# Kernel optimization log

Hardware: AMD Instinct MI355X
Metric: run time of the kernel (lower is better)

Reference implementation:

```python
import jax, jax.numpy as jnp
import numpy as np

B, T, DM, H, DH = 4, 2048, 1024, 16, 64
DI = H * DH
CLIP = 1.0
LN_EPS = 1e-5


def setup_inputs() -> dict:
    key = jax.random.key(0)
    ks = jax.random.split(key, 9)

    def xav(k, shape):  # xavier_uniform, fan_in=shape[1], fan_out=shape[0]
        lim = float(np.sqrt(6.0 / (shape[0] + shape[1])))
        return jax.random.uniform(k, shape, jnp.float32, -lim, lim)

    def kai(k, shape):  # default nn.Linear weight init
        lim = float(1.0 / np.sqrt(shape[1]))
        return jax.random.uniform(k, shape, jnp.float32, -lim, lim)

    return {
        "x": jax.random.normal(ks[0], (B, T, DM), jnp.float32),
        "Wq": xav(ks[1], (DI, DM)),
        "Wk": xav(ks[2], (DI, DM)),
        "Wv": xav(ks[3], (DI, DM)),
        "Wa": kai(ks[4], (DI, DM)), "ba": jnp.full((DI,), 3.0, jnp.float32),
        "Wb": kai(ks[5], (H, DM)), "bb": jnp.zeros((H,), jnp.float32),
        "Wg": kai(ks[6], (H, DM)), "bg": jnp.zeros((H,), jnp.float32),
        "WaR": kai(ks[7], (DI, DM)), "baR": jnp.full((DI,), 3.0, jnp.float32),
        "Wo": xav(ks[8], (DM, DI)),
        "ln_w": jnp.ones((DM,), jnp.float32),
        "ln_b": jnp.zeros((DM,), jnp.float32),
    }


def reference(x, Wq, Wk, Wv, Wa, ba, Wb, bb, Wg, bg, WaR, baR, Wo, ln_w, ln_b):
    Bs, Ts, _ = x.shape
    residual = x
    # LayerNorm
    mu = jnp.mean(x, -1, keepdims=True)
    var = jnp.mean((x - mu) ** 2, -1, keepdims=True)
    xn = (x - mu) / jnp.sqrt(var + LN_EPS) * ln_w + ln_b

    q = (xn @ Wq.T).reshape(Bs, Ts, H, DH)
    k = (xn @ Wk.T).reshape(Bs, Ts, H, DH)
    v = (xn @ Wv.T).reshape(Bs, Ts, H, DH)
    alpha = jax.nn.sigmoid(xn @ Wa.T + ba).reshape(Bs, Ts, H, DH)
    aR = jax.nn.sigmoid(xn @ WaR.T + baR).reshape(Bs, Ts, H, DH)
    beta = jax.nn.sigmoid(xn @ Wb.T + bb)   # (B,T,H)
    gamma = jax.nn.sigmoid(xn @ Wg.T + bg)  # (B,T,H)

    tm = lambda a: jnp.moveaxis(a, 1, 0)  # time-major for scan
    xs = (tm(q), tm(k), tm(v), tm(alpha), tm(aR), tm(beta), tm(gamma))
    S0 = jnp.zeros((Bs, H, DH, DH), x.dtype)

    def step(carry, inp):
        S, R = carry
        q_t, k_t, v_t, a_t, aR_t, b_t, g_t = inp  # (B,H,d) / (B,H)
        kn = k_t / jnp.maximum(jnp.linalg.norm(k_t, axis=-1, keepdims=True), 1e-12)
        # residual target from previous state: r = clip(v - S^T k)
        pred = jnp.einsum('bhji,bhj->bhi', S, kn)
        r = jnp.clip(v_t - pred, -CLIP, CLIP)
        # primary state: S = diag(alpha) S; S += beta k (v - k^T S)
        S = a_t[..., None] * S
        kp = jnp.einsum('bhd,bhde->bhe', kn, S)
        S = S + b_t[..., None, None] * kn[..., None] * (v_t - kp)[..., None, :]
        o = jnp.einsum('bhji,bhj->bhi', S, q_t)
        # residual state
        R = aR_t[..., None] * R
        kpR = jnp.einsum('bhd,bhde->bhe', kn, R)
        R = R + g_t[..., None, None] * kn[..., None] * (r - kpR)[..., None, :]
        o = o + jnp.einsum('bhji,bhj->bhi', R, q_t)
        return (S, R), o

    _, os = jax.lax.scan(step, (S0, S0), xs)  # os: (T,B,H,d)
    out = jnp.moveaxis(os, 0, 1).reshape(Bs, Ts, DI) @ Wo.T
    return out + residual  # dropout is identity at inference
```

## Files before the change

### kernel.cpp

```cpp
#include <hip/hip_runtime.h>
#include <hip/hip_fp16.h>

#define B_SZ 4
#define T_SEQ 2048
#define NH 16
#define HD 64
#define DMODEL 1024
#define MTOT (B_SZ * T_SEQ)

typedef __bf16 bf16x8 __attribute__((ext_vector_type(8)));
typedef float f32x4 __attribute__((ext_vector_type(4)));
typedef float f32x2 __attribute__((ext_vector_type(2)));
typedef _Float16 f16x4 __attribute__((ext_vector_type(4)));

__device__ __forceinline__ unsigned short f2bf(float f) {
    union { float f; unsigned int i; } c; c.f = f;
    unsigned int u = c.i;
    u += 0x7fffu + ((u >> 16) & 1u);
    return (unsigned short)(u >> 16);
}
__device__ __forceinline__ float sigm(float x) { return 1.f / (1.f + __expf(-x)); }

__device__ __forceinline__ void dma16(const void* g, void* l) {
    __builtin_amdgcn_global_load_lds(
        (const __attribute__((address_space(1))) void*)g,
        (__attribute__((address_space(3))) void*)l, 16, 0, 0);
}

template <int CTRL>
__device__ __forceinline__ float dppadd(float x) {
    int v = __builtin_amdgcn_update_dpp(0, __builtin_bit_cast(int, x), CTRL, 0xf, 0xf, false);
    return x + __builtin_bit_cast(float, v);
}
__device__ __forceinline__ float rowsum16(float x) {
    x = dppadd<0x128>(x);
    x = dppadd<0x124>(x);
    x = dppadd<0x122>(x);
    x = dppadd<0x121>(x);
    return x;
}

__device__ __forceinline__ void rowsum3(float& a, float& b, float& c) {
    asm volatile(
        "s_nop 1\n\t"
        "v_add_f32_dpp %0, %0, %0 row_ror:8 row_mask:0xf bank_mask:0xf\n\t"
        "v_add_f32_dpp %1, %1, %1 row_ror:8 row_mask:0xf bank_mask:0xf\n\t"
        "v_add_f32_dpp %2, %2, %2 row_ror:8 row_mask:0xf bank_mask:0xf\n\t"
        "v_add_f32_dpp %0, %0, %0 row_ror:4 row_mask:0xf bank_mask:0xf\n\t"
        "v_add_f32_dpp %1, %1, %1 row_ror:4 row_mask:0xf bank_mask:0xf\n\t"
        "v_add_f32_dpp %2, %2, %2 row_ror:4 row_mask:0xf bank_mask:0xf\n\t"
        "v_add_f32_dpp %0, %0, %0 row_ror:2 row_mask:0xf bank_mask:0xf\n\t"
        "v_add_f32_dpp %1, %1, %1 row_ror:2 row_mask:0xf bank_mask:0xf\n\t"
        "v_add_f32_dpp %2, %2, %2 row_ror:2 row_mask:0xf bank_mask:0xf\n\t"
        "v_add_f32_dpp %0, %0, %0 row_ror:1 row_mask:0xf bank_mask:0xf\n\t"
        "v_add_f32_dpp %1, %1, %1 row_ror:1 row_mask:0xf bank_mask:0xf\n\t"
        "v_add_f32_dpp %2, %2, %2 row_ror:1 row_mask:0xf bank_mask:0xf"
        : "+v"(a), "+v"(b), "+v"(c));
}

__global__ __launch_bounds__(256, 1) void k_ln(const float* __restrict__ x,
                                               const float* __restrict__ lnw,
                                               const float* __restrict__ lnb,
                                               unsigned short* __restrict__ xn) {
    const int m = blockIdx.x;
    const int t = threadIdx.x;
    float4 xv = ((const float4*)(x + (size_t)m * DMODEL))[t];
    float s = xv.x + xv.y + xv.z + xv.w;
    float s2 = xv.x * xv.x + xv.y * xv.y + xv.z * xv.z + xv.w * xv.w;
#pragma unroll
    for (int off = 32; off >= 1; off >>= 1) {
        s += __shfl_xor(s, off);
        s2 += __shfl_xor(s2, off);
    }
    __shared__ float red[8];
    const int wid = t >> 6;
    if ((t & 63) == 0) { red[wid] = s; red[4 + wid] = s2; }
    __syncthreads();
    if (t == 0) {
        float su = red[0] + red[1] + red[2] + red[3];
        float sq = red[4] + red[5] + red[6] + red[7];
        float mu = su * (1.f / DMODEL);
        float var = sq * (1.f / DMODEL) - mu * mu;
        red[0] = mu;
        red[1] = rsqrtf(var + 1e-5f);
    }
    __syncthreads();
    float mu = red[0], rstd = red[1];
    float4 w4 = ((const float4*)lnw)[t];
    float4 b4 = ((const float4*)lnb)[t];
    ushort4 o;
    o.x = f2bf((xv.x - mu) * rstd * w4.x + b4.x);
    o.y = f2bf((xv.y - mu) * rstd * w4.y + b4.y);
    o.z = f2bf((xv.z - mu) * rstd * w4.z + b4.z);
    o.w = f2bf((xv.w - mu) * rstd * w4.w + b4.w);
    ((ushort4*)(xn + (size_t)m * DMODEL))[t] = o;
}

struct WPtrs { const float* p0; const float* p1; const float* p2; const float* p3; const float* p4; };

__global__ __launch_bounds__(256, 1) void k_wconv(WPtrs w, unsigned short* __restrict__ dst) {
    const int plane = blockIdx.y;
    const float* src = plane == 0 ? w.p0 : plane == 1 ? w.p1 : plane == 2 ? w.p2
                                                             : plane == 3 ? w.p3 : w.p4;
    const size_t i = ((size_t)blockIdx.x * 256 + threadIdx.x) * 8;
    float4 f0 = *(const float4*)(src + i);
    float4 f1 = *(const float4*)(src + i + 4);
    uint4 o;
    o.x = (unsigned)f2bf(f0.x) | ((unsigned)f2bf(f0.y) << 16);
    o.y = (unsigned)f2bf(f0.z) | ((unsigned)f2bf(f0.w) << 16);
    o.z = (unsigned)f2bf(f1.x) | ((unsigned)f2bf(f1.y) << 16);
    o.w = (unsigned)f2bf(f1.z) | ((unsigned)f2bf(f1.w) << 16);
    *(uint4*)(dst + (size_t)plane * 1048576 + i) = o;
}

__global__ __launch_bounds__(256, 1) void k_cvt1(const float* __restrict__ src,
                                                 unsigned short* __restrict__ dst) {
    const size_t i = ((size_t)blockIdx.x * 256 + threadIdx.x) * 8;
    float4 f0 = *(const float4*)(src + i);
    float4 f1 = *(const float4*)(src + i + 4);
    uint4 o;
    o.x = (unsigned)f2bf(f0.x) | ((unsigned)f2bf(f0.y) << 16);
    o.y = (unsigned)f2bf(f0.z) | ((unsigned)f2bf(f0.w) << 16);
    o.z = (unsigned)f2bf(f1.x) | ((unsigned)f2bf(f1.y) << 16);
    o.w = (unsigned)f2bf(f1.z) | ((unsigned)f2bf(f1.w) << 16);
    *(uint4*)(dst + i) = o;
}

template <int KDIM>
__device__ __forceinline__ void gemm128(const unsigned short* __restrict__ A,
                                        const unsigned short* __restrict__ Bw,
                                        int m0, int n0, f32x4 acc[4][4]) {
    __shared__ __align__(16) unsigned short sA[3 * 128 * 32];
    __shared__ __align__(16) unsigned short sB[3 * 128 * 32];

    const int t = threadIdx.x;
    const int lane = t & 63;
    const int wv = t >> 6;
    const int wm = wv >> 1, wn = wv & 1;
    const int ml = lane & 15, kq = lane >> 4;

#pragma unroll
    for (int i = 0; i < 4; i++)
#pragma unroll
        for (int j = 0; j < 4; j++) {
            f32x4 z; z[0] = 0.f; z[1] = 0.f; z[2] = 0.f; z[3] = 0.f;
            acc[i][j] = z;
        }

    const unsigned short* pA = A + (size_t)m0 * KDIM;
    const unsigned short* pB = Bw + (size_t)n0 * KDIM;
    const unsigned short* gA0 = pA + (size_t)(t >> 2) * KDIM + (t & 3) * 8;
    const unsigned short* gA1 = gA0 + (size_t)64 * KDIM;
    const unsigned short* gB0 = pB + (size_t)(t >> 2) * KDIM + (t & 3) * 8;
    const unsigned short* gB1 = gB0 + (size_t)64 * KDIM;
    unsigned short* lA0 = sA + wv * 512;
    unsigned short* lA1 = lA0 + 2048;
    unsigned short* lB0 = sB + wv * 512;
    unsigned short* lB1 = lB0 + 2048;

    constexpr int NK = KDIM / 32;

#pragma unroll
    for (int p = 0; p < 3; p++) {
        const int ko = p * 32, bo = p * 4096;
        dma16(gA0 + ko, lA0 + bo);
        dma16(gA1 + ko, lA1 + bo);
        dma16(gB0 + ko, lB0 + bo);
        dma16(gB1 + ko, lB1 + bo);
    }

    int bi = 0;
    for (int kb = 0; kb < NK; kb++) {
        if (kb + 2 < NK)
            asm volatile("s_waitcnt vmcnt(8)" ::: "memory");
        else if (kb + 1 < NK)
            asm volatile("s_waitcnt vmcnt(4)" ::: "memory");
        else
            asm volatile("s_waitcnt vmcnt(0)" ::: "memory");
        __builtin_amdgcn_s_barrier();

        const int bo = bi * 4096;
        const unsigned short* bA = sA + bo;
        const unsigned short* bB = sB + bo;
        bf16x8 af[4], bfr[4];
#pragma unroll
        for (int mt = 0; mt < 4; mt++)
            af[mt] = *(const bf16x8*)&bA[(wm * 64 + mt * 16 + ml) * 32 + kq * 8];
#pragma unroll
        for (int nt = 0; nt < 4; nt++)
            bfr[nt] = *(const bf16x8*)&bB[(wn * 64 + nt * 16 + ml) * 32 + kq * 8];
        asm volatile("s_waitcnt lgkmcnt(0)" ::: "memory");
        __builtin_amdgcn_s_barrier();

        if (kb + 3 < NK) {
            const int ko = (kb + 3) * 32;
            dma16(gA0 + ko, lA0 + bo);
            dma16(gA1 + ko, lA1 + bo);
            dma16(gB0 + ko, lB0 + bo);
            dma16(gB1 + ko, lB1 + bo);
        }
#pragma unroll
        for (int mt = 0; mt < 4; mt++)
#pragma unroll
            for (int nt = 0; nt < 4; nt++)
                acc[mt][nt] = __builtin_amdgcn_mfma_f32_16x16x32_bf16(af[mt], bfr[nt], acc[mt][nt], 0, 0, 0);
        bi = (bi == 2) ? 0 : bi + 1;
    }
}

template <typename OT>
__global__ __launch_bounds__(256, 2) void k_proj(const unsigned short* __restrict__ xn,
                                                 const unsigned short* __restrict__ wbf,
                                                 const float* __restrict__ ba,
                                                 const float* __restrict__ baR,
                                                 OT* __restrict__ qo, OT* __restrict__ ko,
                                                 OT* __restrict__ vo, OT* __restrict__ ao,
                                                 OT* __restrict__ aRo) {
    const int m0 = blockIdx.x * 128;
    const int yt = blockIdx.y;
    const int widx = yt >> 3;
    const int n0 = (yt & 7) * 128;
    const unsigned short* W = wbf + (size_t)widx * 1048576;
    f32x4 acc[4][4];
    gemm128<1024>(xn, W, m0, n0, acc);

    OT* outp = widx == 0 ? qo : widx == 1 ? ko : widx == 2 ? vo : widx == 3 ? ao : aRo;
    const float* bias = (widx == 3) ? ba : (widx == 4) ? baR : (const float*)0;
    const int lane = threadIdx.x & 63;
    const int wv = threadIdx.x >> 6;
    const int wm = wv >> 1, wn = wv & 1;
    const int ml = lane & 15, kq = lane >> 4;
#pragma unroll
    for (int mt = 0; mt < 4; mt++)
#pragma unroll
        for (int nt = 0; nt < 4; nt++) {
            const int rowg = m0 + wm * 64 + mt * 16 + kq * 4;
            const int colg = n0 + wn * 64 + nt * 16 + ml;
            float bval = bias ? bias[colg] : 0.f;
#pragma unroll
            for (int r = 0; r < 4; r++) {
                float v = acc[mt][nt][r];
                if (widx >= 3) v = sigm(v + bval);
                outp[(size_t)(rowg + r) * DMODEL + colg] = (OT)v;
            }
        }
}

__global__ __launch_bounds__(256, 1) void k_bg(const unsigned short* __restrict__ xn,
                                               const float* __restrict__ Wb,
                                               const float* __restrict__ bb,
                                               const float* __restrict__ Wg,
                                               const float* __restrict__ bgp,
                                               f32x2* __restrict__ bgpk) {
    const int m = blockIdx.x;
    const int t = threadIdx.x;
    const int h = t >> 4, seg = t & 15;
    const ushort4* xr = (const ushort4*)(xn + (size_t)m * DMODEL + seg * 64);
    const float4* wbr = (const float4*)(Wb + (size_t)h * DMODEL + seg * 64);
    const float4* wgr = (const float4*)(Wg + (size_t)h * DMODEL + seg * 64);
    float db = 0.f, dg = 0.f;
#pragma unroll
    for (int u = 0; u < 16; u++) {
        ushort4 a = xr[u];
        float4 w1 = wbr[u], w2 = wgr[u];
        union { unsigned int i; float f; } c0, c1, c2, c3;
        c0.i = ((unsigned int)a.x) << 16; c1.i = ((unsigned int)a.y) << 16;
        c2.i = ((unsigned int)a.z) << 16; c3.i = ((unsigned int)a.w) << 16;
        db += c0.f * w1.x + c1.f * w1.y + c2.f * w1.z + c3.f * w1.w;
        dg += c0.f * w2.x + c1.f * w2.y + c2.f * w2.z + c3.f * w2.w;
    }
#pragma unroll
    for (int off = 1; off < 16; off <<= 1) {
        db += __shfl_xor(db, off);
        dg += __shfl_xor(dg, off);
    }
    if (seg == 0) {
        f32x2 o;
        o[0] = sigm(db + bb[h]);
        o[1] = sigm(dg + bgp[h]);
        bgpk[(size_t)m * NH + h] = o;
    }
}

__global__ __launch_bounds__(256, 1) void k_prep16(__half* __restrict__ kb) {
    const int row = blockIdx.x * 16 + (threadIdx.x >> 4);
    const int tr = threadIdx.x & 15;
    const int bh = row >> 11, t = row & 2047;
    const size_t idx = ((size_t)((bh >> 4) * T_SEQ + t)) * DMODEL + (bh & 15) * 64 + tr * 4;
    f16x4 k4 = *(const f16x4*)((const __half*)kb + idx);
    float k0 = (float)k4[0], k1 = (float)k4[1], k2 = (float)k4[2], k3 = (float)k4[3];
    float ss = k0 * k0 + k1 * k1 + k2 * k2 + k3 * k3;
    ss = rowsum16(ss);
    float inv = 1.f / fmaxf(sqrtf(ss), 1e-12f);
    f16x4 o;
    o[0] = (_Float16)(k0 * inv); o[1] = (_Float16)(k1 * inv);
    o[2] = (_Float16)(k2 * inv); o[3] = (_Float16)(k3 * inv);
    *(f16x4*)(kb + idx) = o;
}

__global__ __launch_bounds__(256, 1) void k_prep32(float* __restrict__ kb) {
    const int row = blockIdx.x * 16 + (threadIdx.x >> 4);
    const int tr = threadIdx.x & 15;
    const int bh = row >> 11, t = row & 2047;
    const size_t idx = ((size_t)((bh >> 4) * T_SEQ + t)) * DMODEL + (bh & 15) * 64 + tr * 4;
    f32x4 k4 = *(const f32x4*)(kb + idx);
    float ss = k4[0] * k4[0] + k4[1] * k4[1] + k4[2] * k4[2] + k4[3] * k4[3];
    ss = rowsum16(ss);
    float inv = 1.f / fmaxf(sqrtf(ss), 1e-12f);
    f32x4 o;
    o[0] = k4[0] * inv; o[1] = k4[1] * inv; o[2] = k4[2] * inv; o[3] = k4[3] * inv;
    *(f32x4*)(kb + idx) = o;
}

__global__ __attribute__((amdgpu_flat_work_group_size(256, 256), amdgpu_waves_per_eu(1, 1)))
void k_scan32(const float* __restrict__ qb,
              const float* __restrict__ knb,
              const float* __restrict__ vb,
              const float* __restrict__ ab,
              const float* __restrict__ aRb,
              const f32x2* __restrict__ bgpk,
              unsigned short* __restrict__ ob) {
    const int blk = blockIdx.x;
    const int bh = blk & 63, cg = blk >> 6;
    const int b = bh >> 4, h = bh & 15;
    const int t = threadIdx.x;
    const int col = t >> 4, tr = t & 15;
    const int ii = cg * 16 + col;
    const int j0 = tr * 4;

    const size_t blkoff = (size_t)b * T_SEQ * DMODEL + h * 64;
    const float* pq = qb + blkoff;
    const float* pk = knb + blkoff;
    const float* pa = ab + blkoff;
    const float* pr = aRb + blkoff;
    const float* pvb = vb + blkoff;
    const f32x2* pbg = bgpk + (size_t)b * T_SEQ * NH + h;
    unsigned short* obp = ob + blkoff + ii;

    f32x2 S01 = {0.f, 0.f}, S23 = {0.f, 0.f}, R01 = {0.f, 0.f}, R23 = {0.f, 0.f};

    f32x4 rk[6], rq[6], ra[6], rr[6];
    float rv[6];
    f32x2 rbg[6];

#pragma unroll
    for (int p = 0; p < 6; p++) {
        const size_t vo = (size_t)p * DMODEL;
        rk[p] = *(const f32x4*)(pk + vo + j0);
        rq[p] = *(const f32x4*)(pq + vo + j0);
        ra[p] = *(const f32x4*)(pa + vo + j0);
        rr[p] = *(const f32x4*)(pr + vo + j0);
        rv[p] = pvb[vo + ii];
        rbg[p] = pbg[(size_t)p * NH];
    }

    float oA, oB, oC;

#define SCAN_BODY32(P, ODEST)                                                       \
    {                                                                               \
        const f32x2 kn01 = {rk[P][0], rk[P][1]}, kn23 = {rk[P][2], rk[P][3]};       \
        const f32x2 a01 = {ra[P][0], ra[P][1]}, a23 = {ra[P][2], ra[P][3]};         \
        const f32x2 x01 = {rr[P][0], rr[P][1]}, x23 = {rr[P][2], rr[P][3]};         \
        const f32x2 q01 = {rq[P][0], rq[P][1]}, q23 = {rq[P][2], rq[P][3]};         \
        const float vc = rv[P];                                                     \
        const float beta = rbg[P][0], gamma = rbg[P][1];                            \
        const f32x2 Sd01 = a01 * S01, Sd23 = a23 * S23;                             \
        const f32x2 Rd01 = x01 * R01, Rd23 = x23 * R23;                             \
        const f32x2 pv2 = S01 * kn01 + S23 * kn23;                                  \
        const f32x2 kp2 = Sd01 * kn01 + Sd23 * kn23;                                \
        const f32x2 kR2 = Rd01 * kn01 + Rd23 * kn23;                                \
        float pred = pv2[0] + pv2[1];                                               \
        float kp = kp2[0] + kp2[1];                                                 \
        float kpR = kR2[0] + kR2[1];                                                \
        rowsum3(pred, kp, kpR);                                                     \
        const float rres = fminf(fmaxf(vc - pred, -1.f), 1.f);                      \
        const float cS = beta * (vc - kp);                                          \
        const float cR = gamma * (rres - kpR);                                      \
        const f32x2 cS2 = {cS, cS}, cR2 = {cR, cR};                                 \
        S01 = cS2 * kn01 + Sd01; S23 = cS2 * kn23 + Sd23;                           \
        R01 = cR2 * kn01 + Rd01; R23 = cR2 * kn23 + Rd23;                           \
        const f32x2 ov = (S01 + R01) * q01 + (S23 + R23) * q23;                     \
        ODEST = ov[0] + ov[1];                                                      \
              \
        {                                                                           \
            const int sp = (st + (P) + 6) & (T_SEQ - 1);                            \
            const size_t vo = (size_t)sp * DMODEL;                                  \
            rk[P] = *(const f32x4*)(pk + vo + j0);                                  \
            rq[P] = *(const f32x4*)(pq + vo + j0);                                  \
            ra[P] = *(const f32x4*)(pa + vo + j0);                                  \
            rr[P] = *(const f32x4*)(pr + vo + j0);                                  \
            rv[P] = pvb[vo + ii];                                                   \
            rbg[P] = pbg[(size_t)sp * NH];                                          \
        }                                                                           \
    }

#define FLUSH3(SBASE)                                                               \
    {                                                                               \
        rowsum3(oA, oB, oC);                                                        \
        if (tr == 0) {                                                              \
            if ((SBASE) < T_SEQ)     obp[(size_t)(SBASE) * DMODEL] = f2bf(oA);      \
            if ((SBASE) + 1 < T_SEQ) obp[(size_t)((SBASE) + 1) * DMODEL] = f2bf(oB);\
            if ((SBASE) + 2 < T_SEQ) obp[(size_t)((SBASE) + 2) * DMODEL] = f2bf(oC);\
        }                                                                           \
    }

    for (int st = 0; st < T_SEQ; st += 6) {
        SCAN_BODY32(0, oA)
        SCAN_BODY32(1, oB)
        SCAN_BODY32(2, oC)
        FLUSH3(st)
        SCAN_BODY32(3, oA)
        SCAN_BODY32(4, oB)
        SCAN_BODY32(5, oC)
        FLUSH3(st + 3)
    }
#undef SCAN_BODY32
#undef FLUSH3
}

__global__ __launch_bounds__(256, 1) void k_scan16(const __half* __restrict__ qb,
                                                   const __half* __restrict__ knb,
                                                   const __half* __restrict__ vb,
                                                   const __half* __restrict__ ab,
                                                   const __half* __restrict__ aRb,
                                                   const f32x2* __restrict__ bgpk,
                                                   unsigned short* __restrict__ ob) {
    const int blk = blockIdx.x;
    const int bh = blk & 63, cg = blk >> 6;
    const int b = bh >> 4, h = bh & 15;
    const int t = threadIdx.x;
    const int col = t >> 4, tr = t & 15;
    const int ii = cg * 16 + col;
    const int j0 = tr * 4;

    const size_t vecbase = ((size_t)b * T_SEQ) * DMODEL + h * 64 + j0;
    const size_t vbase = ((size_t)b * T_SEQ) * DMODEL + h * 64 + ii;
    const size_t bgbase = ((size_t)b * T_SEQ) * NH + h;

    const __half* pk = knb + vecbase;
    const __half* pq = qb + vecbase;
    const __half* pa = ab + vecbase;
    const __half* pr = aRb + vecbase;

    float S0 = 0, S1 = 0, S2 = 0, S3 = 0, R0 = 0, R1 = 0, R2 = 0, R3 = 0;

    f16x4 rk[6], rq[6], ra[6], rr[6];
    __half rv[6];
    f32x2 rbg[6];
    f32x4 fkn[6], fq[6], fa[6], fr[6];
    float fv[6];

#pragma unroll
    for (int p = 0; p < 6; p++) {
        const size_t voff = (size_t)p * DMODEL;
        rk[p] = *(const f16x4*)(pk + voff);
        rq[p] = *(const f16x4*)(pq + voff);
        ra[p] = *(const f16x4*)(pa + voff);
        rr[p] = *(const f16x4*)(pr + voff);
        rv[p] = vb[vbase + voff];
        rbg[p] = bgpk[bgbase + (size_t)p * NH];
    }
    fkn[0][0] = (float)rk[0][0]; fkn[0][1] = (float)rk[0][1]; fkn[0][2] = (float)rk[0][2]; fkn[0][3] = (float)rk[0][3];
    fq[0][0] = (float)rq[0][0]; fq[0][1] = (float)rq[0][1]; fq[0][2] = (float)rq[0][2]; fq[0][3] = (float)rq[0][3];
    fa[0][0] = (float)ra[0][0]; fa[0][1] = (float)ra[0][1]; fa[0][2] = (float)ra[0][2]; fa[0][3] = (float)ra[0][3];
    fr[0][0] = (float)rr[0][0]; fr[0][1] = (float)rr[0][1]; fr[0][2] = (float)rr[0][2]; fr[0][3] = (float)rr[0][3];
    fv[0] = (float)rv[0];

#define SCAN_BODY(P, PN)                                                              \
    {                                                                                 \
        const int s = st + (P);                                                       \
        const float beta = rbg[P][0], gamma = rbg[P][1];                              \
        {                                                                             \
            const size_t voff = (size_t)((s + 6) & (T_SEQ - 1)) * DMODEL;             \
            rk[P] = *(const f16x4*)(pk + voff);                                       \
            rq[P] = *(const f16x4*)(pq + voff);                                       \
            ra[P] = *(const f16x4*)(pa + voff);                                       \
            rr[P] = *(const f16x4*)(pr + voff);                                       \
            rv[P] = vb[vbase + voff];                                                 \
        }                                                                             \
        fkn[PN][0] = (float)rk[PN][0]; fkn[PN][1] = (float)rk[PN][1];                 \
        fkn[PN][2] = (float)rk[PN][2]; fkn[PN][3] = (float)rk[PN][3];                 \
        fq[PN][0] = (float)rq[PN][0]; fq[PN][1] = (float)rq[PN][1];                   \
        fq[PN][2] = (float)rq[PN][2]; fq[PN][3] = (float)rq[PN][3];                   \
        fa[PN][0] = (float)ra[PN][0]; fa[PN][1] = (float)ra[PN][1];                   \
        fa[PN][2] = (float)ra[PN][2]; fa[PN][3] = (float)ra[PN][3];                   \
        fr[PN][0] = (float)rr[PN][0]; fr[PN][1] = (float)rr[PN][1];                   \
        fr[PN][2] = (float)rr[PN][2]; fr[PN][3] = (float)rr[PN][3];                   \
        fv[PN] = (float)rv[PN];                                                       \
        {                                                                             \
            const float kn0 = fkn[P][0], kn1 = fkn[P][1], kn2 = fkn[P][2], kn3 = fkn[P][3]; \
            const float a0 = fa[P][0], a1 = fa[P][1], a2 = fa[P][2], a3 = fa[P][3];   \
            const float x0 = fr[P][0], x1 = fr[P][1], x2 = fr[P][2], x3 = fr[P][3];   \
            const float vc = fv[P];                                                   \
            float pred = S0 * kn0 + S1 * kn1 + S2 * kn2 + S3 * kn3;                   \
            float Sd0 = a0 * S0, Sd1 = a1 * S1, Sd2 = a2 * S2, Sd3 = a3 * S3;         \
            float Rd0 = x0 * R0, Rd1 = x1 * R1, Rd2 = x2 * R2, Rd3 = x3 * R3;         \
            float kp = Sd0 * kn0 + Sd1 * kn1 + Sd2 * kn2 + Sd3 * kn3;                 \
            float kpR = Rd0 * kn0 + Rd1 * kn1 + Rd2 * kn2 + Rd3 * kn3;                \
            pred = rowsum16(pred);                                                    \
            kp = rowsum16(kp);                                                        \
            kpR = rowsum16(kpR);                                                      \
            const float rres = fminf(fmaxf(vc - pred, -1.f), 1.f);                    \
            const float cS = beta * (vc - kp);                                        \
            const float cR = gamma * (rres - kpR);                                    \
            S0 = fmaf(cS, kn0, Sd0); S1 = fmaf(cS, kn1, Sd1);                         \
            S2 = fmaf(cS, kn2, Sd2); S3 = fmaf(cS, kn3, Sd3);                         \
            R0 = fmaf(cR, kn0, Rd0); R1 = fmaf(cR, kn1, Rd1);                         \
            R2 = fmaf(cR, kn2, Rd2); R3 = fmaf(cR, kn3, Rd3);                         \
            float o = (S0 + R0) * fq[P][0] + (S1 + R1) * fq[P][1] +                   \
                      (S2 + R2) * fq[P][2] + (S3 + R3) * fq[P][3];                    \
            o = rowsum16(o);                                                          \
            if (tr == 0 && s < T_SEQ)                                                 \
                ob[vbase + (size_t)s * DMODEL] = f2bf(o);                             \
        }                                                                             \
        rbg[P] = bgpk[bgbase + (size_t)((s + 6) & (T_SEQ - 1)) * NH];                 \
    }

    for (int st = 0; st < T_SEQ; st += 6) {
        SCAN_BODY(0, 1)
        SCAN_BODY(1, 2)
        SCAN_BODY(2, 3)
        SCAN_BODY(3, 4)
        SCAN_BODY(4, 5)
        SCAN_BODY(5, 0)
    }
#undef SCAN_BODY
}

__global__ __launch_bounds__(256, 2) void k_out(const unsigned short* __restrict__ ob,
                                                const unsigned short* __restrict__ wobf,
                                                const float* __restrict__ x,
                                                float* __restrict__ out) {
    const int m0 = blockIdx.x * 128;
    const int n0 = blockIdx.y * 128;
    f32x4 acc[4][4];
    gemm128<1024>(ob, wobf, m0, n0, acc);
    const int lane = threadIdx.x & 63;
    const int wv = threadIdx.x >> 6;
    const int wm = wv >> 1, wn = wv & 1;
    const int ml = lane & 15, kq = lane >> 4;
#pragma unroll
    for (int mt = 0; mt < 4; mt++)
#pragma unroll
        for (int nt = 0; nt < 4; nt++) {
            const int rowg = m0 + wm * 64 + mt * 16 + kq * 4;
            const int colg = n0 + wn * 64 + nt * 16 + ml;
#pragma unroll
            for (int r = 0; r < 4; r++) {
                size_t idx = (size_t)(rowg + r) * DMODEL + colg;
                out[idx] = acc[mt][nt][r] + x[idx];
            }
        }
}

extern "C" void kernel_launch(void* const* d_in, const int* in_sizes, int n_in,
                              void* d_out, int out_size, void* d_ws, size_t ws_size,
                              hipStream_t stream) {
    const float* x = (const float*)d_in[0];
    const float* Wq = (const float*)d_in[1];
    const float* Wk = (const float*)d_in[2];
    const float* Wv = (const float*)d_in[3];
    const float* Wa = (const float*)d_in[4];
    const float* ba = (const float*)d_in[5];
    const float* Wb = (const float*)d_in[6];
    const float* bb = (const float*)d_in[7];
    const float* Wg = (const float*)d_in[8];
    const float* bg = (const float*)d_in[9];
    const float* WaR = (const float*)d_in[10];
    const float* baR = (const float*)d_in[11];
    const float* Wo = (const float*)d_in[12];
    const float* lnw = (const float*)d_in[13];
    const float* lnb = (const float*)d_in[14];

    const size_t SZH = 16777216ULL;
    const size_t SZF = 33554432ULL;
    const size_t need32 = 5 * SZF + SZH + 2097152ULL;
    const size_t need16 = 6 * SZH + 2097152ULL;

    char* ws = (char*)d_ws;
    unsigned short* wbf = (unsigned short*)d_out;
    WPtrs wp{Wq, Wk, Wv, Wa, WaR};

    if (ws_size >= need32) {
        float* qb = (float*)(ws + 0 * SZF);
        float* kb = (float*)(ws + 1 * SZF);
        float* vb = (float*)(ws + 2 * SZF);
        float* ab = (float*)(ws + 3 * SZF);
        float* aRb = (float*)(ws + 4 * SZF);
        unsigned short* xn = (unsigned short*)(ws + 5 * SZF);
        f32x2* bgpk = (f32x2*)(ws + 5 * SZF + SZH);
        unsigned short* wobf = (unsigned short*)qb;

        k_wconv<<<dim3(512, 5), dim3(256), 0, stream>>>(wp, wbf);
        k_ln<<<dim3(MTOT), dim3(256), 0, stream>>>(x, lnw, lnb, xn);
        k_proj<float><<<dim3(64, 40), dim3(256), 0, stream>>>(xn, wbf, ba, baR, qb, kb, vb, ab, aRb);
        k_bg<<<dim3(MTOT), dim3(256), 0, stream>>>(xn, Wb, bb, Wg, bg, bgpk);
        k_prep32<<<dim3(MTOT * NH / 16), dim3(256), 0, stream>>>(kb);
        k_scan32<<<dim3(256), dim3(256), 0, stream>>>(qb, kb, vb, ab, aRb, bgpk, xn);
        k_cvt1<<<dim3(512), dim3(256), 0, stream>>>(Wo, wobf);
        k_out<<<dim3(64, 8), dim3(256), 0, stream>>>(xn, wobf, x, (float*)d_out);
    } else if (ws_size >= need16) {
        __half* qb = (__half*)(ws + 0 * SZH);
        __half* kb = (__half*)(ws + 1 * SZH);
        __half* vb = (__half*)(ws + 2 * SZH);
        __half* ab = (__half*)(ws + 3 * SZH);
        __half* aRb = (__half*)(ws + 4 * SZH);
        unsigned short* xn = (unsigned short*)(ws + 5 * SZH);
        f32x2* bgpk = (f32x2*)(ws + 6 * SZH);
        unsigned short* wobf = (unsigned short*)qb;

        k_wconv<<<dim3(512, 5), dim3(256), 0, stream>>>(wp, wbf);
        k_ln<<<dim3(MTOT), dim3(256), 0, stream>>>(x, lnw, lnb, xn);
        k_proj<_Float16><<<dim3(64, 40), dim3(256), 0, stream>>>(
            xn, wbf, ba, baR, (_Float16*)qb, (_Float16*)kb, (_Float16*)vb, (_Float16*)ab, (_Float16*)aRb);
        k_bg<<<dim3(MTOT), dim3(256), 0, stream>>>(xn, Wb, bb, Wg, bg, bgpk);
        k_prep16<<<dim3(MTOT * NH / 16), dim3(256), 0, stream>>>(kb);
        k_scan16<<<dim3(256), dim3(256), 0, stream>>>(qb, kb, vb, ab, aRb, bgpk, xn);
        k_cvt1<<<dim3(512), dim3(256), 0, stream>>>(Wo, wobf);
        k_out<<<dim3(64, 8), dim3(256), 0, stream>>>(xn, wobf, x, (float*)d_out);
    }
}
```

Baseline: 798.9 us.

## Use 64-wide K tiles with double buffering and XOR-swizzled LDS layout in GEMM

The shared bf16 GEMM now stages K in 64-element tiles with two buffers instead of 32-element tiles with three. It also XOR-swizzles the 16-byte column chunks in LDS to avoid bank conflicts on the fragment reads. This halves the number of barrier/wait iterations per K loop and doubles the MFMA work per sync. In exchange, the prefetch runs one stage ahead instead of two, which may expose more load latency.

```diff
diff --git a/kernel.cpp b/kernel.cpp
--- a/kernel.cpp
+++ b/kernel.cpp
@@ -130,8 +130,8 @@
 __device__ __forceinline__ void gemm128(const unsigned short* __restrict__ A,
                                         const unsigned short* __restrict__ Bw,
                                         int m0, int n0, f32x4 acc[4][4]) {
-    __shared__ __align__(16) unsigned short sA[3 * 128 * 32];
-    __shared__ __align__(16) unsigned short sB[3 * 128 * 32];
+    __shared__ __align__(16) unsigned short sA[2 * 128 * 64];
+    __shared__ __align__(16) unsigned short sB[2 * 128 * 64];
 
     const int t = threadIdx.x;
     const int lane = t & 63;
@@ -149,62 +149,74 @@
 
     const unsigned short* pA = A + (size_t)m0 * KDIM;
     const unsigned short* pB = Bw + (size_t)n0 * KDIM;
-    const unsigned short* gA0 = pA + (size_t)(t >> 2) * KDIM + (t & 3) * 8;
-    const unsigned short* gA1 = gA0 + (size_t)64 * KDIM;
-    const unsigned short* gB0 = pB + (size_t)(t >> 2) * KDIM + (t & 3) * 8;
-    const unsigned short* gB1 = gB0 + (size_t)64 * KDIM;
-    unsigned short* lA0 = sA + wv * 512;
-    unsigned short* lA1 = lA0 + 2048;
-    unsigned short* lB0 = sB + wv * 512;
-    unsigned short* lB1 = lB0 + 2048;
-
-    constexpr int NK = KDIM / 32;
-
-#pragma unroll
-    for (int p = 0; p < 3; p++) {
-        const int ko = p * 32, bo = p * 4096;
-        dma16(gA0 + ko, lA0 + bo);
-        dma16(gA1 + ko, lA1 + bo);
-        dma16(gB0 + ko, lB0 + bo);
-        dma16(gB1 + ko, lB1 + bo);
-    }
-
-    int bi = 0;
+
+    const unsigned short* gA[4];
+    const unsigned short* gB[4];
+    int lo[4];
+#pragma unroll
+    for (int r = 0; r < 4; r++) {
+        const int slot = r * 256 + t;
+        const int row = slot >> 3;
+        const int cs = (slot & 7) ^ (row & 7);
+        gA[r] = pA + (size_t)row * KDIM + cs * 8;
+        gB[r] = pB + (size_t)row * KDIM + cs * 8;
+        lo[r] = r * 2048 + wv * 512;
+    }
+
+    constexpr int NK = KDIM / 64;
+
+#pragma unroll
+    for (int p = 0; p < 2; p++) {
+        const int ko = p * 64, bo = p * 8192;
+#pragma unroll
+        for (int r = 0; r < 4; r++) {
+            dma16(gA[r] + ko, sA + bo + lo[r]);
+            dma16(gB[r] + ko, sB + bo + lo[r]);
+        }
+    }
+
+    const int m7 = ml & 7;
+
     for (int kb = 0; kb < NK; kb++) {
-        if (kb + 2 < NK)
+        if (kb + 1 < NK)
             asm volatile("s_waitcnt vmcnt(8)" ::: "memory");
-        else if (kb + 1 < NK)
-            asm volatile("s_waitcnt vmcnt(4)" ::: "memory");
         else
             asm volatile("s_waitcnt vmcnt(0)" ::: "memory");
         __builtin_amdgcn_s_barrier();
 
-        const int bo = bi * 4096;
+        const int bo = (kb & 1) * 8192;
         const unsigned short* bA = sA + bo;
         const unsigned short* bB = sB + bo;
-        bf16x8 af[4], bfr[4];
-#pragma unroll
-        for (int mt = 0; mt < 4; mt++)
-            af[mt] = *(const bf16x8*)&bA[(wm * 64 + mt * 16 + ml) * 32 + kq * 8];
-#pragma unroll
-        for (int nt = 0; nt < 4; nt++)
-            bfr[nt] = *(const bf16x8*)&bB[(wn * 64 + nt * 16 + ml) * 32 + kq * 8];
+        bf16x8 af[2][4], bfr[2][4];
+#pragma unroll
+        for (int half = 0; half < 2; half++) {
+            const int cr = ((half << 2) + kq) ^ m7;
+#pragma unroll
+            for (int mt = 0; mt < 4; mt++)
+                af[half][mt] = *(const bf16x8*)&bA[(wm * 64 + mt * 16 + ml) * 64 + cr * 8];
+#pragma unroll
+            for (int nt = 0; nt < 4; nt++)
+                bfr[half][nt] = *(const bf16x8*)&bB[(wn * 64 + nt * 16 + ml) * 64 + cr * 8];
+        }
         asm volatile("s_waitcnt lgkmcnt(0)" ::: "memory");
         __builtin_amdgcn_s_barrier();
 
-        if (kb + 3 < NK) {
-            const int ko = (kb + 3) * 32;
-            dma16(gA0 + ko, lA0 + bo);
-            dma16(gA1 + ko, lA1 + bo);
-            dma16(gB0 + ko, lB0 + bo);
-            dma16(gB1 + ko, lB1 + bo);
+        if (kb + 2 < NK) {
+            const int ko = (kb + 2) * 64;
+#pragma unroll
+            for (int r = 0; r < 4; r++) {
+                dma16(gA[r] + ko, sA + bo + lo[r]);
+                dma16(gB[r] + ko, sB + bo + lo[r]);
+            }
         }
 #pragma unroll
-        for (int mt = 0; mt < 4; mt++)
-#pragma unroll
-            for (int nt = 0; nt < 4; nt++)
-                acc[mt][nt] = __builtin_amdgcn_mfma_f32_16x16x32_bf16(af[mt], bfr[nt], acc[mt][nt], 0, 0, 0);
-        bi = (bi == 2) ? 0 : bi + 1;
+        for (int half = 0; half < 2; half++)
+#pragma unroll
+            for (int mt = 0; mt < 4; mt++)
+#pragma unroll
+                for (int nt = 0; nt < 4; nt++)
+                    acc[mt][nt] = __builtin_amdgcn_mfma_f32_16x16x32_bf16(
+                        af[half][mt], bfr[half][nt], acc[mt][nt], 0, 0, 0);
     }
 }
 
```

Measured after the change: 800.7 us. No clear change (+0.2%).
